# Kernel tuning notes

Hardware: AMD Instinct MI355X
Metric: run time of the kernel (lower is better)

Reference implementation:

```python
import jax, jax.numpy as jnp
import numpy as np

D_MODEL = 512
N_HEADS = 8
D_FF = 2048
E_LAYERS = 2
ENC_IN = 7
MARK_IN = 4
SEQ_LEN = 1536
PRED_LEN = 512
DEC_LEN = 768
BATCH = 8
BUCKET_SIZE = 4
N_HASHES = 4
L_TOTAL = SEQ_LEN + PRED_LEN  # 2048, multiple of 2*bucket_size
DH = D_MODEL // N_HEADS
N_BUCKETS = L_TOTAL // BUCKET_SIZE  # 512
SELF_ATTN_VALUE = -5e4  # reformer_pytorch TOKEN_SELF_ATTN_VALUE


def layernorm(x, g, b, eps=1e-5):
    mu = x.mean(-1, keepdims=True)
    var = ((x - mu) ** 2).mean(-1, keepdims=True)
    return (x - mu) * jax.lax.rsqrt(var + eps) * g + b


def lsh_attention(qk, v, rotations):
    # qk, v: [BH, L, dh]; rotations: [dh, n_hashes, n_buckets//2]
    BH, L, dh = qk.shape
    # --- hashing: argmax over [rotated, -rotated] ---
    rotated = jnp.einsum('bld,dhr->bhlr', qk, rotations)
    rotated = jnp.concatenate([rotated, -rotated], axis=-1)          # [BH,nh,L,nb]
    buckets = jnp.argmax(rotated, axis=-1).astype(jnp.int32)         # [BH,nh,L]
    offsets = (jnp.arange(N_HASHES, dtype=jnp.int32) * N_BUCKETS)[None, :, None]
    buckets = (buckets + offsets).reshape(BH, N_HASHES * L)
    # --- sort by (bucket, time) ---
    ticker = jnp.arange(N_HASHES * L, dtype=jnp.int32)
    buckets_and_t = buckets * L + (ticker % L)
    sticker = jnp.argsort(buckets_and_t, axis=-1).astype(jnp.int32)  # stable
    undo_sort = jnp.argsort(sticker, axis=-1)
    st = sticker % L                                                 # original positions
    sqk = jnp.take_along_axis(qk, st[..., None], axis=1)
    sv = jnp.take_along_axis(v, st[..., None], axis=1)
    # --- chunk: n_chunks = n_hashes * n_buckets, bucket_size per chunk ---
    n_chunks = N_HASHES * N_BUCKETS
    bq_t = st.reshape(BH, n_chunks, BUCKET_SIZE)
    bqk = sqk.reshape(BH, n_chunks, BUCKET_SIZE, dh)
    bv = sv.reshape(BH, n_chunks, BUCKET_SIZE, dh)
    bq = bqk
    bk = bqk / jnp.maximum(jnp.linalg.norm(bqk, axis=-1, keepdims=True), 1e-12)
    look = lambda x: jnp.concatenate([x, jnp.roll(x, 1, axis=1)], axis=2)  # look one chunk back
    bk, bve, bkv_t = look(bk), look(bv), look(bq_t)
    dots = jnp.einsum('bcie,bcje->bcij', bq, bk) * (dh ** -0.5)
    self_mask = bq_t[:, :, :, None] == bkv_t[:, :, None, :]
    dots = jnp.where(self_mask, SELF_ATTN_VALUE, dots)
    lse = jax.nn.logsumexp(dots, axis=-1, keepdims=True)
    probs = jnp.exp(dots - lse)
    bo = jnp.einsum('bcij,bcje->bcie', probs, bve)
    # --- unsort and combine hash rounds via logit weighting ---
    so = bo.reshape(BH, N_HASHES * L, dh)
    slog = lse.reshape(BH, N_HASHES * L)
    o = jnp.take_along_axis(so, undo_sort[..., None], axis=1)
    logits = jnp.take_along_axis(slog, undo_sort, axis=1)
    o = o.reshape(BH, N_HASHES, L, dh)
    logits = logits.reshape(BH, N_HASHES, L, 1)
    w = jax.nn.softmax(logits, axis=1)
    return (o * w).sum(axis=1)  # [BH, L, dh]


def split_heads(x, B, L):
    return x.reshape(B, L, N_HEADS, DH).transpose(0, 2, 1, 3).reshape(B * N_HEADS, L, DH)


def _forward(x_enc, x_mark_enc, x_dec, x_mark_dec, token_w, temp_w, qk_w, v_w, out_w, out_b,
             ln1_g, ln1_b, ff1_w, ff1_b, ff2_w, ff2_b, ln2_g, ln2_b, norm_g, norm_b,
             proj_w, proj_b, rotations):
    x = jnp.concatenate([x_enc, x_dec[:, -PRED_LEN:, :]], axis=1)        # [B,L,enc_in]
    xm = jnp.concatenate([x_mark_enc, x_mark_dec[:, -PRED_LEN:, :]], axis=1)
    B, L, _ = x.shape
    # TokenEmbedding: Conv1d(enc_in, d_model, k=3, circular, no bias)
    xp = jnp.concatenate([x[:, -1:], x, x[:, :1]], axis=1)               # circular pad 1
    val = sum(jnp.einsum('blc,dc->bld', xp[:, k:k + L], token_w[:, :, k]) for k in range(3))
    # PositionalEmbedding (sinusoidal)
    pos = jnp.arange(L, dtype=jnp.float32)[:, None]
    div = jnp.exp(jnp.arange(0, D_MODEL, 2, dtype=jnp.float32) * (-np.log(10000.0) / D_MODEL))
    pe = jnp.zeros((L, D_MODEL), jnp.float32)
    pe = pe.at[:, 0::2].set(jnp.sin(pos * div)).at[:, 1::2].set(jnp.cos(pos * div))
    # TimeFeatureEmbedding: Linear(4, d_model, no bias)
    h = val + xm @ temp_w.T + pe[None]
    for l in range(E_LAYERS):
        qk = split_heads(h @ qk_w[l].T, B, L)
        v = split_heads(h @ v_w[l].T, B, L)
        attn = lsh_attention(qk, v, rotations[l])
        attn = attn.reshape(B, N_HEADS, L, DH).transpose(0, 2, 1, 3).reshape(B, L, D_MODEL)
        attn = attn @ out_w[l].T + out_b[l]
        h = h + attn
        y = h = layernorm(h, ln1_g[l], ln1_b[l])
        y = jax.nn.gelu(y @ ff1_w[l].T + ff1_b[l], approximate=False)
        y = y @ ff2_w[l].T + ff2_b[l]
        h = layernorm(h + y, ln2_g[l], ln2_b[l])
    h = layernorm(h, norm_g, norm_b)
    dec_out = h @ proj_w.T + proj_b                                      # [B, L, 1]
    return dec_out[:, -PRED_LEN:][..., None]                             # [B, pred_len, 1, 1]


def setup_inputs() -> dict:
    key = jax.random.key(0)
    ks = iter(jax.random.split(key, 32))
    rn = lambda shape, s=0.02: jax.random.normal(next(ks), shape, jnp.float32) * s
    inp = {
        'x_enc': jax.random.normal(next(ks), (BATCH, SEQ_LEN, ENC_IN), jnp.float32),
        'x_mark_enc': jax.random.normal(next(ks), (BATCH, SEQ_LEN, MARK_IN), jnp.float32),
        'x_dec': jax.random.normal(next(ks), (BATCH, DEC_LEN, ENC_IN), jnp.float32),
        'x_mark_dec': jax.random.normal(next(ks), (BATCH, DEC_LEN, MARK_IN), jnp.float32),
        'token_w': rn((D_MODEL, ENC_IN, 3), 0.1),
        'temp_w': rn((D_MODEL, MARK_IN), 0.1),
        'qk_w': rn((E_LAYERS, D_MODEL, D_MODEL)),
        'v_w': rn((E_LAYERS, D_MODEL, D_MODEL)),
        'out_w': rn((E_LAYERS, D_MODEL, D_MODEL)),
        'out_b': jnp.zeros((E_LAYERS, D_MODEL), jnp.float32),
        'ln1_g': jnp.ones((E_LAYERS, D_MODEL), jnp.float32),
        'ln1_b': jnp.zeros((E_LAYERS, D_MODEL), jnp.float32),
        'ff1_w': rn((E_LAYERS, D_FF, D_MODEL)),
        'ff1_b': jnp.zeros((E_LAYERS, D_FF), jnp.float32),
        'ff2_w': rn((E_LAYERS, D_MODEL, D_FF)),
        'ff2_b': jnp.zeros((E_LAYERS, D_MODEL), jnp.float32),
        'ln2_g': jnp.ones((E_LAYERS, D_MODEL), jnp.float32),
        'ln2_b': jnp.zeros((E_LAYERS, D_MODEL), jnp.float32),
        'norm_g': jnp.ones((D_MODEL,), jnp.float32),
        'norm_b': jnp.zeros((D_MODEL,), jnp.float32),
        'proj_w': rn((1, D_MODEL)),
        'proj_b': jnp.zeros((1,), jnp.float32),
        'rotations': jax.random.normal(next(ks), (E_LAYERS, DH, N_HASHES, N_BUCKETS // 2), jnp.float32),
    }
    return inp


def reference(x_enc, x_mark_enc, x_dec, x_mark_dec, token_w, temp_w, qk_w, v_w, out_w, out_b,
              ln1_g, ln1_b, ff1_w, ff1_b, ff2_w, ff2_b, ln2_g, ln2_b, norm_g, norm_b,
              proj_w, proj_b, rotations):
    return _forward(x_enc, x_mark_enc, x_dec, x_mark_dec, token_w, temp_w, qk_w, v_w, out_w, out_b,
                    ln1_g, ln1_b, ff1_w, ff1_b, ff2_w, ff2_b, ln2_g, ln2_b, norm_g, norm_b,
                    proj_w, proj_b, rotations)
```

## Files before the change

kernel.cpp:

```cpp
#include <hip/hip_runtime.h>
#include <math.h>

#define BATCH 8
#define LTOT 2048
#define DM 512
#define NHEADS 8
#define DH 64
#define NBH 64
#define NHASH 4
#define SEQ 1536
#define DECL 768
#define DFF 2048
#define NCH 2048

typedef unsigned short u16;
typedef unsigned int u32;
typedef unsigned long long u64;
typedef __attribute__((ext_vector_type(8))) short short8;
typedef __attribute__((ext_vector_type(4))) float floatx4;

static __device__ __forceinline__ double gelu_d(double x) {
    return 0.5 * x * (1.0 + erf(x * 0.70710678118654752440));
}

static __device__ __forceinline__ u16 f2bf(float x) {
    u32 u = __float_as_uint(x);
    return (u16)((u + 0x7fffu + ((u >> 16) & 1u)) >> 16);
}
static __device__ __forceinline__ float bf2f(u16 h) {
    return __uint_as_float(((u32)h) << 16);
}
static __device__ __forceinline__ void split3(float x, u16& h, u16& m, u16& l) {
    h = f2bf(x);
    float r1 = x - bf2f(h);
    m = f2bf(r1);
    l = f2bf(r1 - bf2f(m));
}
static __device__ __forceinline__ u32 ordf(float x) {
    u32 b = __float_as_uint(x);
    return (b & 0x80000000u) ? ~b : (b | 0x80000000u);
}
static __device__ __forceinline__ u32 pack_hi16(u32 a, u32 b) {
    return __builtin_amdgcn_perm(b, a, 0x07060302u);
}
static __device__ __forceinline__ void tsplit3_pack(
    float x0, float x1, u32& ph, u32& pm, u32& pl)
{
    u32 b0 = __float_as_uint(x0), b1 = __float_as_uint(x1);
    ph = pack_hi16(b0, b1);
    float r0 = x0 - __uint_as_float(b0 & 0xFFFF0000u);
    float r1 = x1 - __uint_as_float(b1 & 0xFFFF0000u);
    u32 c0 = __float_as_uint(r0), c1 = __float_as_uint(r1);
    pm = pack_hi16(c0, c1);
    float s0 = r0 - __uint_as_float(c0 & 0xFFFF0000u);
    float s1 = r1 - __uint_as_float(c1 & 0xFFFF0000u);
    pl = pack_hi16(__float_as_uint(s0), __float_as_uint(s1));
}
static __device__ __forceinline__ void tsplit2_pack(
    float x0, float x1, u32& ph, u32& pm)
{
    u32 b0 = __float_as_uint(x0), b1 = __float_as_uint(x1);
    ph = pack_hi16(b0, b1);
    float r0 = x0 - __uint_as_float(b0 & 0xFFFF0000u);
    float r1 = x1 - __uint_as_float(b1 & 0xFFFF0000u);
    pm = pack_hi16(__float_as_uint(r0), __float_as_uint(r1));
}

__global__ __launch_bounds__(512) void build_h_kernel(
    const float* __restrict__ x_enc, const float* __restrict__ x_mark_enc,
    const float* __restrict__ x_dec, const float* __restrict__ x_mark_dec,
    const float* __restrict__ token_w, const float* __restrict__ temp_w,
    float* __restrict__ H)
{
    int bl = blockIdx.x;
    int b = bl >> 11, l = bl & 2047;
    __shared__ float xr[3][7];
    __shared__ float xmr[4];
    int tid = threadIdx.x;
    if (tid < 21) {
        int k = tid / 7, c = tid % 7;
        int t = (l + k - 1 + LTOT) & 2047;
        float v;
        if (t < SEQ) v = x_enc[(b * SEQ + t) * 7 + c];
        else         v = x_dec[(b * DECL + (t - 1280)) * 7 + c];
        xr[k][c] = v;
    } else if (tid < 25) {
        int m = tid - 21;
        float v;
        if (l < SEQ) v = x_mark_enc[(b * SEQ + l) * 4 + m];
        else         v = x_mark_dec[(b * DECL + (l - 1280)) * 4 + m];
        xmr[m] = v;
    }
    __syncthreads();
    int d = tid;
    double val = 0.0;
    #pragma unroll
    for (int k = 0; k < 3; ++k)
        #pragma unroll
        for (int c = 0; c < 7; ++c)
            val += (double)xr[k][c] * (double)token_w[(d * 7 + c) * 3 + k];
    double tmp = 0.0;
    #pragma unroll
    for (int m = 0; m < 4; ++m) tmp += (double)xmr[m] * (double)temp_w[d * 4 + m];
    const float cf = (float)(-9.210340371976184 / 512.0);
    float ef  = (float)(2 * (d >> 1)) * cf;
    float dvf = (float)exp((double)ef);
    float angf = (float)l * dvf;
    double pe = (d & 1) ? cos((double)angf) : sin((double)angf);
    H[((size_t)b * LTOT + l) * DM + d] = (float)(val + tmp + pe);
}

__global__ __launch_bounds__(256) void wsplit_kernel(
    const float* __restrict__ qkw, const float* __restrict__ vw,
    const float* __restrict__ ow, const float* __restrict__ f1w,
    const float* __restrict__ f2w,
    u16* __restrict__ Ph, u16* __restrict__ Pm, u16* __restrict__ Pl)
{
    size_t i = ((size_t)blockIdx.x * 256 + threadIdx.x) * 4;
    const float* src; size_t off, base; int kshift;
    if (i < 262144)       { src = qkw; off = i;           base = 0;       kshift = 9; }
    else if (i < 524288)  { src = vw;  off = i - 262144;  base = 262144;  kshift = 9; }
    else if (i < 786432)  { src = ow;  off = i - 524288;  base = 524288;  kshift = 9; }
    else if (i < 1835008) { src = f1w; off = i - 786432;  base = 786432;  kshift = 9; }
    else                  { src = f2w; off = i - 1835008; base = 1835008; kshift = 11; }
    int K = 1 << kshift;
    int n  = (int)(off >> kshift);
    int kg = (int)(off & (size_t)(K - 1));
    int nt = n >> 7, r = n & 127, kt = kg >> 5, kk = kg & 31;
    size_t o = base + ((((size_t)nt * (K >> 5) + kt) << 12) | ((size_t)r << 5) | kk);
    float4 x = *(const float4*)(src + off);
    u32 h01, m01, l01, h23, m23, l23;
    tsplit3_pack(x.x, x.y, h01, m01, l01);
    tsplit3_pack(x.z, x.w, h23, m23, l23);
    *(uint2*)(Ph + o) = make_uint2(h01, h23);
    *(uint2*)(Pm + o) = make_uint2(m01, m23);
    *(uint2*)(Pl + o) = make_uint2(l01, l23);
}

template<int NSPLIT>
__global__ __launch_bounds__(256) void gemm_mfma(
    const float* __restrict__ A,
    const u16* __restrict__ WTh, const u16* __restrict__ WTm,
    const u16* __restrict__ WTl,
    const float* __restrict__ bias, const float* __restrict__ res,
    float* __restrict__ C, int M, int N, int K, int act)
{
    __shared__ u16 Ah[128][32], Am[128][32], Al[128][32];
    __shared__ u16 Wh[128][32], Wm[128][32], Wl[128][32];
    const int tid = threadIdx.x;
    const int n0 = blockIdx.x * 128, m0 = blockIdx.y * 128;
    const int row = tid >> 1;
    const int koff = (tid & 1) * 16;
    const float* Ag = A + (size_t)(m0 + row) * K + koff;

    const int wv = tid >> 6, lane = tid & 63;
    const int m0w = (wv >> 1) * 64, n0w = (wv & 1) * 64;
    const int fr = lane & 15, quad = lane >> 4;
    u16* WhF = &Wh[0][0]; u16* WmF = &Wm[0][0]; u16* WlF = &Wl[0][0];

    floatx4 acc[4][4];
    #pragma unroll
    for (int i = 0; i < 4; ++i)
        #pragma unroll
        for (int j = 0; j < 4; ++j) acc[i][j] = (floatx4)0.0f;

    for (int kt = 0; kt < K; kt += 32) {
        const size_t tb = ((size_t)blockIdx.x * (K >> 5) + (kt >> 5)) * 4096;
        uint4 wh0 = *(const uint4*)(WTh + tb + tid * 8);
        uint4 wh1 = *(const uint4*)(WTh + tb + 2048 + tid * 8);
        uint4 wm0 = *(const uint4*)(WTm + tb + tid * 8);
        uint4 wm1 = *(const uint4*)(WTm + tb + 2048 + tid * 8);
        uint4 wl0, wl1;
        if (NSPLIT == 3) {
            wl0 = *(const uint4*)(WTl + tb + tid * 8);
            wl1 = *(const uint4*)(WTl + tb + 2048 + tid * 8);
        }
        u32 pah[8], pam[8], pal[8];
        #pragma unroll
        for (int g = 0; g < 4; ++g) {
            float4 a4 = *(const float4*)(Ag + kt + g * 4);
            if (NSPLIT == 3) {
                tsplit3_pack(a4.x, a4.y, pah[g*2], pam[g*2], pal[g*2]);
                tsplit3_pack(a4.z, a4.w, pah[g*2+1], pam[g*2+1], pal[g*2+1]);
            } else {
                tsplit2_pack(a4.x, a4.y, pah[g*2], pam[g*2]);
                tsplit2_pack(a4.z, a4.w, pah[g*2+1], pam[g*2+1]);
            }
        }
        __syncthreads();
        ((uint4*)&Ah[row][koff])[0] = make_uint4(pah[0], pah[1], pah[2], pah[3]);
        ((uint4*)&Ah[row][koff])[1] = make_uint4(pah[4], pah[5], pah[6], pah[7]);
        ((uint4*)&Am[row][koff])[0] = make_uint4(pam[0], pam[1], pam[2], pam[3]);
        ((uint4*)&Am[row][koff])[1] = make_uint4(pam[4], pam[5], pam[6], pam[7]);
        *(uint4*)(WhF + tid * 8) = wh0;
        *(uint4*)(WhF + 2048 + tid * 8) = wh1;
        *(uint4*)(WmF + tid * 8) = wm0;
        *(uint4*)(WmF + 2048 + tid * 8) = wm1;
        if (NSPLIT == 3) {
            ((uint4*)&Al[row][koff])[0] = make_uint4(pal[0], pal[1], pal[2], pal[3]);
            ((uint4*)&Al[row][koff])[1] = make_uint4(pal[4], pal[5], pal[6], pal[7]);
            *(uint4*)(WlF + tid * 8) = wl0;
            *(uint4*)(WlF + 2048 + tid * 8) = wl1;
        }
        __syncthreads();
        short8 ah4[4], am4[4], al4[4];
        #pragma unroll
        for (int rt = 0; rt < 4; ++rt) {
            int r = m0w + rt * 16 + fr;
            ah4[rt] = *(const short8*)&Ah[r][quad * 8];
            am4[rt] = *(const short8*)&Am[r][quad * 8];
            if (NSPLIT == 3) al4[rt] = *(const short8*)&Al[r][quad * 8];
        }
        #pragma unroll
        for (int ct = 0; ct < 4; ++ct) {
            int nrw = n0w + ct * 16 + fr;
            short8 bh4 = *(const short8*)&Wh[nrw][quad * 8];
            short8 bm4 = *(const short8*)&Wm[nrw][quad * 8];
            short8 bl4;
            if (NSPLIT == 3) bl4 = *(const short8*)&Wl[nrw][quad * 8];
            #pragma unroll
            for (int rt = 0; rt < 4; ++rt) {
                floatx4 c = acc[rt][ct];
                c = __builtin_amdgcn_mfma_f32_16x16x32_bf16(ah4[rt], bh4, c, 0, 0, 0);
                c = __builtin_amdgcn_mfma_f32_16x16x32_bf16(ah4[rt], bm4, c, 0, 0, 0);
                c = __builtin_amdgcn_mfma_f32_16x16x32_bf16(am4[rt], bh4, c, 0, 0, 0);
                if (NSPLIT == 3) {
                    c = __builtin_amdgcn_mfma_f32_16x16x32_bf16(ah4[rt], bl4, c, 0, 0, 0);
                    c = __builtin_amdgcn_mfma_f32_16x16x32_bf16(am4[rt], bm4, c, 0, 0, 0);
                    c = __builtin_amdgcn_mfma_f32_16x16x32_bf16(al4[rt], bh4, c, 0, 0, 0);
                }
                acc[rt][ct] = c;
            }
        }
    }
    #pragma unroll
    for (int rt = 0; rt < 4; ++rt) {
        #pragma unroll
        for (int ct = 0; ct < 4; ++ct) {
            int n = n0 + n0w + ct * 16 + fr;
            #pragma unroll
            for (int reg = 0; reg < 4; ++reg) {
                int m = m0 + m0w + rt * 16 + quad * 4 + reg;
                double v = (double)acc[rt][ct][reg];
                if (bias) v += (double)bias[n];
                if (res)  v += (double)res[(size_t)m * N + n];
                if (act == 1) v = gelu_d(v);
                C[(size_t)m * N + n] = (float)v;
            }
        }
    }
}

__global__ __launch_bounds__(256) void rot_split_kernel(
    const float* __restrict__ rot, u16* __restrict__ RSh,
    u16* __restrict__ RSm, u16* __restrict__ RSl)
{
    int h = blockIdx.x;
    int r = threadIdx.x;
    #pragma unroll 4
    for (int d = 0; d < 64; ++d) {
        float v = rot[(d * 4 + h) * 256 + r];
        u16 hh, mm, ll;
        split3(v, hh, mm, ll);
        size_t o = ((size_t)h * 256 + r) * 64 + d;
        RSh[o] = hh; RSm[o] = mm; RSl[o] = ll;
    }
}

__global__ __launch_bounds__(256) void lsh_hash_mfma(
    const float* __restrict__ QK, const u16* __restrict__ RSh,
    const u16* __restrict__ RSm, const u16* __restrict__ RSl,
    int* __restrict__ BKT)
{
    __shared__ u16 Ah[128][72], Am[128][72], Al[128][72];
    __shared__ u64 best[128];
    int bid = blockIdx.x;
    int tt = bid & 15;
    int h  = (bid >> 4) & 3;
    int bh = bid >> 6;
    int tid = threadIdx.x;
    int b = bh >> 3, hd = bh & 7;
    const int t0 = tt * 128;

    if (tid < 128) best[tid] = 0ull;

    {
        int row = tid >> 1;
        int kbase = (tid & 1) * 32;
        const float* src = QK + ((size_t)(b * LTOT + t0 + row)) * DM + hd * DH + kbase;
        u32 ph[16], pm[16], pl[16];
        #pragma unroll
        for (int g = 0; g < 8; ++g) {
            float4 a4 = *(const float4*)(src + g * 4);
            u16 h0, m0_, l0, h1, m1_, l1;
            split3(a4.x, h0, m0_, l0); split3(a4.y, h1, m1_, l1);
            ph[g*2]   = (u32)h0 | ((u32)h1 << 16);
            pm[g*2]   = (u32)m0_ | ((u32)m1_ << 16);
            pl[g*2]   = (u32)l0 | ((u32)l1 << 16);
            split3(a4.z, h0, m0_, l0); split3(a4.w, h1, m1_, l1);
            ph[g*2+1] = (u32)h0 | ((u32)h1 << 16);
            pm[g*2+1] = (u32)m0_ | ((u32)m1_ << 16);
            pl[g*2+1] = (u32)l0 | ((u32)l1 << 16);
        }
        #pragma unroll
        for (int g = 0; g < 4; ++g) {
            ((uint4*)&Ah[row][kbase])[g] = make_uint4(ph[g*4], ph[g*4+1], ph[g*4+2], ph[g*4+3]);
            ((uint4*)&Am[row][kbase])[g] = make_uint4(pm[g*4], pm[g*4+1], pm[g*4+2], pm[g*4+3]);
            ((uint4*)&Al[row][kbase])[g] = make_uint4(pl[g*4], pl[g*4+1], pl[g*4+2], pl[g*4+3]);
        }
    }
    __syncthreads();

    const int wv = tid >> 6, lane = tid & 63;
    const int fr = lane & 15, quad = lane >> 4;
    const int nbase = wv * 64;

    floatx4 acc[8][4];
    #pragma unroll
    for (int i = 0; i < 8; ++i)
        #pragma unroll
        for (int j = 0; j < 4; ++j) acc[i][j] = (floatx4)0.0f;

    #pragma unroll
    for (int kt = 0; kt < 2; ++kt) {
        #pragma unroll
        for (int ct = 0; ct < 4; ++ct) {
            size_t bo = ((size_t)h * 256 + nbase + ct * 16 + fr) * 64 + kt * 32 + quad * 8;
            short8 bh4 = *(const short8*)(RSh + bo);
            short8 bm4 = *(const short8*)(RSm + bo);
            short8 bl4 = *(const short8*)(RSl + bo);
            #pragma unroll
            for (int rt = 0; rt < 8; ++rt) {
                const int ar = rt * 16 + fr, ak = kt * 32 + quad * 8;
                short8 ah4 = *(const short8*)&Ah[ar][ak];
                short8 am4 = *(const short8*)&Am[ar][ak];
                short8 al4 = *(const short8*)&Al[ar][ak];
                floatx4 c = acc[rt][ct];
                c = __builtin_amdgcn_mfma_f32_16x16x32_bf16(ah4, bh4, c, 0, 0, 0);
                c = __builtin_amdgcn_mfma_f32_16x16x32_bf16(ah4, bm4, c, 0, 0, 0);
                c = __builtin_amdgcn_mfma_f32_16x16x32_bf16(am4, bh4, c, 0, 0, 0);
                c = __builtin_amdgcn_mfma_f32_16x16x32_bf16(ah4, bl4, c, 0, 0, 0);
                c = __builtin_amdgcn_mfma_f32_16x16x32_bf16(am4, bm4, c, 0, 0, 0);
                c = __builtin_amdgcn_mfma_f32_16x16x32_bf16(al4, bh4, c, 0, 0, 0);
                acc[rt][ct] = c;
            }
        }
    }

    #pragma unroll
    for (int rt = 0; rt < 8; ++rt) {
        #pragma unroll
        for (int reg = 0; reg < 4; ++reg) {
            u64 key = 0ull;
            #pragma unroll
            for (int ct = 0; ct < 4; ++ct) {
                float v = acc[rt][ct][reg];
                u32 idxp = nbase + ct * 16 + fr;
                u32 idxn = idxp + 256;
                u64 kp = ((u64)ordf(v) << 32) | (u32)(0xFFFFFFFFu - idxp);
                u64 kn = ((u64)ordf(-v) << 32) | (u32)(0xFFFFFFFFu - idxn);
                if (kp > key) key = kp;
                if (kn > key) key = kn;
            }
            #pragma unroll
            for (int m = 1; m <= 8; m <<= 1) {
                u64 o = __shfl_xor((unsigned long long)key, m, 64);
                if (o > key) key = o;
            }
            if (fr == 0) {
                int tok = rt * 16 + quad * 4 + reg;
                atomicMax(&best[tok], key);
            }
        }
    }
    __syncthreads();
    if (tid < 128) {
        u32 idx = 0xFFFFFFFFu - (u32)best[tid];
        BKT[((size_t)bh * NHASH + h) * LTOT + t0 + tid] = (int)idx;
    }
}

__global__ __launch_bounds__(256) void lsh_sort_kernel(
    const int* __restrict__ BKT, int* __restrict__ STS)
{
    __shared__ unsigned short bkt[2048];
    __shared__ unsigned int hist2[16][512];
    __shared__ unsigned int bstart[512];
    int bid = blockIdx.x;
    int h = bid & 3, bh = bid >> 2;
    int tid = threadIdx.x;
    const int* src = BKT + ((size_t)bh * NHASH + h) * LTOT;
    for (int t = tid; t < 2048; t += 256) bkt[t] = (unsigned short)src[t];
    for (int i = tid; i < 16 * 512; i += 256) (&hist2[0][0])[i] = 0u;
    __syncthreads();
    for (int t = tid; t < 2048; t += 256)
        atomicAdd(&hist2[t >> 7][bkt[t]], 1u);
    __syncthreads();
    for (int bb = tid; bb < 512; bb += 256) {
        unsigned int run = 0;
        #pragma unroll
        for (int g = 0; g < 16; ++g) {
            unsigned int c = hist2[g][bb];
            hist2[g][bb] = run;
            run += c;
        }
        bstart[bb] = run;
    }
    __syncthreads();
    if (tid == 0) {
        unsigned int run = 0;
        for (int bb = 0; bb < 512; ++bb) {
            unsigned int c = bstart[bb];
            bstart[bb] = run;
            run += c;
        }
    }
    __syncthreads();
    int* dst = STS + (size_t)bh * (NHASH * LTOT) + h * LTOT;
    for (int t = tid; t < 2048; t += 256) {
        int bb = bkt[t];
        unsigned int rank = hist2[t >> 7][bb];
        int g0 = t & ~127;
        for (int u = g0; u < t; ++u) rank += (bkt[u] == (unsigned short)bb);
        dst[bstart[bb] + rank] = t;
    }
}

__global__ __launch_bounds__(256) void attn_lse_kernel(
    const float* __restrict__ QK, const int* __restrict__ STS,
    float* __restrict__ LSE, float* __restrict__ PRB)
{
    int wid = (blockIdx.x * 256 + threadIdx.x) >> 6;
    int lane = threadIdx.x & 63;
    int bh = wid >> 11;
    int c  = wid & 2047;
    int cp = (c + NCH - 1) & (NCH - 1);
    const int* sts = STS + (size_t)bh * 8192;
    int tok[8];
    #pragma unroll
    for (int j = 0; j < 4; ++j) tok[j] = sts[4 * c + j];
    #pragma unroll
    for (int j = 0; j < 4; ++j) tok[4 + j] = sts[4 * cp + j];
    int b = bh >> 3, hd = bh & 7;
    const float* base = QK + ((size_t)b * LTOT) * DM + hd * DH + lane;
    float kd[8];
    #pragma unroll
    for (int j = 0; j < 8; ++j) kd[j] = base[(size_t)tok[j] * DM];
    float rnrm[8];
    #pragma unroll
    for (int j = 0; j < 8; ++j) {
        float v = kd[j] * kd[j];
        #pragma unroll
        for (int m = 32; m; m >>= 1) v += __shfl_xor(v, m, 64);
        rnrm[j] = 0.125f / fmaxf(sqrtf(v), 1e-12f);
    }
    int hr = c >> 9;
    size_t cbase = ((size_t)bh * NCH + c) * 32;
    float pkeep = 0.f;
    #pragma unroll
    for (int i = 0; i < 4; ++i) {
        float dots[8];
        float myd = -5e4f;
        #pragma unroll
        for (int j = 0; j < 8; ++j) {
            float v = kd[i] * kd[j];
            #pragma unroll
            for (int m = 32; m; m >>= 1) v += __shfl_xor(v, m, 64);
            dots[j] = (tok[j] == tok[i]) ? -5e4f : v * rnrm[j];
            if ((lane & 7) == j) myd = dots[j];
        }
        float mx = dots[0];
        #pragma unroll
        for (int j = 1; j < 8; ++j) mx = fmaxf(mx, dots[j]);
        float s = 0.f;
        #pragma unroll
        for (int j = 0; j < 8; ++j) s += expf(dots[j] - mx);
        float pn = expf(myd - mx) / s;
        if ((lane >> 3) == i) pkeep = pn;
        if (lane == 0)
            LSE[((size_t)bh * NHASH + hr) * LTOT + tok[i]] = mx + logf(s);
    }
    if (lane < 32) PRB[cbase + lane] = pkeep;
}

__global__ __launch_bounds__(256) void wsoft_kernel(
    const float* __restrict__ LSE, float* __restrict__ W4)
{
    int idx = blockIdx.x * 256 + threadIdx.x;
    int bh = idx >> 11, t = idx & 2047;
    float L[4];
    #pragma unroll
    for (int hh = 0; hh < 4; ++hh)
        L[hh] = LSE[((size_t)bh * NHASH + hh) * LTOT + t];
    float wm = fmaxf(fmaxf(L[0], L[1]), fmaxf(L[2], L[3]));
    float ws = 0.f;
    #pragma unroll
    for (int hh = 0; hh < 4; ++hh) ws += expf(L[hh] - wm);
    float inv = 1.f / ws;
    #pragma unroll
    for (int hh = 0; hh < 4; ++hh)
        W4[((size_t)bh * NHASH + hh) * LTOT + t] = expf(L[hh] - wm) * inv;
}

__global__ __launch_bounds__(256) void attn_out_kernel(
    const float* __restrict__ V, const int* __restrict__ STS,
    const float* __restrict__ PRB, const float* __restrict__ W4,
    float* __restrict__ C)
{
    int wid = (blockIdx.x * 256 + threadIdx.x) >> 6;
    int lane = threadIdx.x & 63;
    int bh = wid >> 11;
    int c  = wid & 2047;
    int cp = (c + NCH - 1) & (NCH - 1);
    const int* sts = STS + (size_t)bh * 8192;
    int tok[8];
    #pragma unroll
    for (int j = 0; j < 4; ++j) tok[j] = sts[4 * c + j];
    #pragma unroll
    for (int j = 0; j < 4; ++j) tok[4 + j] = sts[4 * cp + j];
    int b = bh >> 3, hd = bh & 7;
    const float* vbase = V + ((size_t)b * LTOT) * DM + hd * DH + lane;
    float vd[8];
    #pragma unroll
    for (int j = 0; j < 8; ++j) vd[j] = vbase[(size_t)tok[j] * DM];
    size_t cbase = ((size_t)bh * NCH + c) * 32;
    float pv = PRB[cbase + (lane & 31)];
    int hr = c >> 9;
    const float* w4b = W4 + ((size_t)bh * NHASH + hr) * LTOT;
    float* crow0 = C + ((size_t)b * LTOT) * DM + hd * DH + lane;
    #pragma unroll
    for (int i = 0; i < 4; ++i) {
        float w = w4b[tok[i]];
        float acc = 0.f;
        #pragma unroll
        for (int j = 0; j < 8; ++j)
            acc += __shfl(pv, i * 8 + j, 64) * vd[j];
        atomicAdd(crow0 + (size_t)tok[i] * DM, acc * w);
    }
}

__global__ __launch_bounds__(256) void ln_kernel(
    const float* __restrict__ X, float* __restrict__ Y,
    const float* __restrict__ g, const float* __restrict__ bta)
{
    int row = blockIdx.x;
    int tid = threadIdx.x;
    const float* x = X + (size_t)row * DM;
    double v0 = (double)x[tid], v1 = (double)x[tid + 256];
    double s = v0 + v1;
    double q = v0 * v0 + v1 * v1;
    #pragma unroll
    for (int off = 32; off; off >>= 1) {
        s += __shfl_down(s, off, 64);
        q += __shfl_down(q, off, 64);
    }
    __shared__ double ss[4], qq[4];
    int wid = tid >> 6, lane = tid & 63;
    if (lane == 0) { ss[wid] = s; qq[wid] = q; }
    __syncthreads();
    if (tid == 0) {
        double S = ss[0] + ss[1] + ss[2] + ss[3];
        double Q = qq[0] + qq[1] + qq[2] + qq[3];
        double mu = S * (1.0 / 512.0);
        double var = Q * (1.0 / 512.0) - mu * mu;
        ss[0] = mu;
        qq[0] = 1.0 / sqrt(var + 1e-5);
    }
    __syncthreads();
    double mu = ss[0], rs = qq[0];
    Y[(size_t)row * DM + tid] =
        (float)((v0 - mu) * rs * (double)g[tid] + (double)bta[tid]);
    Y[(size_t)row * DM + tid + 256] =
        (float)((v1 - mu) * rs * (double)g[tid + 256] + (double)bta[tid + 256]);
}

__global__ __launch_bounds__(64) void proj_kernel(
    const float* __restrict__ Hf, const float* __restrict__ pw,
    const float* __restrict__ pb, float* __restrict__ out)
{
    int idx = blockIdx.x;
    int b = idx >> 9, i = idx & 511;
    const float* row = Hf + ((size_t)(b * LTOT + SEQ + i)) * DM;
    int lane = threadIdx.x;
    double s = 0.0;
    #pragma unroll
    for (int k = 0; k < 8; ++k)
        s += (double)row[lane + 64 * k] * (double)pw[lane + 64 * k];
    #pragma unroll
    for (int off = 32; off; off >>= 1) s += __shfl_down(s, off, 64);
    if (lane == 0) out[idx] = (float)(s + (double)pb[0]);
}

extern "C" void kernel_launch(void* const* d_in, const int* in_sizes, int n_in,
                              void* d_out, int out_size, void* d_ws, size_t ws_size,
                              hipStream_t stream)
{
    const float* x_enc      = (const float*)d_in[0];
    const float* x_mark_enc = (const float*)d_in[1];
    const float* x_dec      = (const float*)d_in[2];
    const float* x_mark_dec = (const float*)d_in[3];
    const float* token_w    = (const float*)d_in[4];
    const float* temp_w     = (const float*)d_in[5];
    const float* qk_w       = (const float*)d_in[6];
    const float* v_w        = (const float*)d_in[7];
    const float* out_w      = (const float*)d_in[8];
    const float* out_b      = (const float*)d_in[9];
    const float* ln1_g      = (const float*)d_in[10];
    const float* ln1_b      = (const float*)d_in[11];
    const float* ff1_w      = (const float*)d_in[12];
    const float* ff1_b      = (const float*)d_in[13];
    const float* ff2_w      = (const float*)d_in[14];
    const float* ff2_b      = (const float*)d_in[15];
    const float* ln2_g      = (const float*)d_in[16];
    const float* ln2_b      = (const float*)d_in[17];
    const float* norm_g     = (const float*)d_in[18];
    const float* norm_b     = (const float*)d_in[19];
    const float* proj_w     = (const float*)d_in[20];
    const float* proj_b     = (const float*)d_in[21];
    const float* rotations  = (const float*)d_in[22];

    float* ws = (float*)d_ws;
    const size_t S = (size_t)BATCH * LTOT * DM;
    float* Hb  = ws;
    float* QKb = ws + S;
    float* Vb  = ws + 2 * S;
    float* Cb  = ws + 3 * S;
    float* Yb  = QKb;
    int*   BKTb = (int*)(ws + 4 * S);
    float* LSEb = ws + 4 * S + 524288;
    int*   STSb = (int*)(ws + 4 * S + 2 * 524288);
    u16*   RShb = (u16*)(ws + 4 * S + 3 * 524288);
    u16*   RSmb = RShb + 4 * 256 * 64;
    u16*   RSlb = RSmb + 4 * 256 * 64;
    const size_t WTOT = 2883584;
    u16*   WPh = (u16*)(ws + 4 * S + 3 * 524288 + 98304);
    u16*   WPm = WPh + WTOT;
    u16*   WPl = WPm + WTOT;
    float* PRBb = ws + 4 * S + 3 * 524288 + 98304 + (3 * WTOT) / 2;
    float* W4b  = PRBb + (size_t)NBH * NCH * 32;
    const size_t WO_QK = 0, WO_V = 262144, WO_O = 524288,
                 WO_F1 = 786432, WO_F2 = 1835008;

    build_h_kernel<<<BATCH * LTOT, 512, 0, stream>>>(
        x_enc, x_mark_enc, x_dec, x_mark_dec, token_w, temp_w, Hb);

    const int M = BATCH * LTOT;
    const int ATT_BLOCKS = NBH * NCH / 4;
    for (int l = 0; l < 2; ++l) {
        const float* qkw = qk_w + (size_t)l * DM * DM;
        const float* vw  = v_w  + (size_t)l * DM * DM;
        const float* ow  = out_w + (size_t)l * DM * DM;
        const float* ob  = out_b + (size_t)l * DM;
        const float* l1g = ln1_g + (size_t)l * DM;
        const float* l1b = ln1_b + (size_t)l * DM;
        const float* f1w = ff1_w + (size_t)l * DFF * DM;
        const float* f1b = ff1_b + (size_t)l * DFF;
        const float* f2w = ff2_w + (size_t)l * DM * DFF;
        const float* f2b = ff2_b + (size_t)l * DM;
        const float* l2g = ln2_g + (size_t)l * DM;
        const float* l2b = ln2_b + (size_t)l * DM;
        const float* rot = rotations + (size_t)l * DH * NHASH * 256;

        wsplit_kernel<<<2816, 256, 0, stream>>>(qkw, vw, ow, f1w, f2w, WPh, WPm, WPl);

        dim3 gQ(DM / 128, M / 128);
        gemm_mfma<3><<<gQ, 256, 0, stream>>>(Hb, WPh + WO_QK, WPm + WO_QK, WPl + WO_QK,
                                             nullptr, nullptr, QKb, M, DM, DM, 0);
        if (l == 0)
            gemm_mfma<3><<<gQ, 256, 0, stream>>>(Hb, WPh + WO_V, WPm + WO_V, WPl + WO_V,
                                                 nullptr, nullptr, Vb, M, DM, DM, 0);
        else
            gemm_mfma<2><<<gQ, 256, 0, stream>>>(Hb, WPh + WO_V, WPm + WO_V, WPl + WO_V,
                                                 nullptr, nullptr, Vb, M, DM, DM, 0);

        rot_split_kernel<<<4, 256, 0, stream>>>(rot, RShb, RSmb, RSlb);
        lsh_hash_mfma<<<NBH * NHASH * 16, 256, 0, stream>>>(QKb, RShb, RSmb, RSlb, BKTb);
        lsh_sort_kernel<<<NBH * NHASH, 256, 0, stream>>>(BKTb, STSb);

        hipMemsetAsync(Cb, 0, S * sizeof(float), stream);
        attn_lse_kernel<<<ATT_BLOCKS, 256, 0, stream>>>(QKb, STSb, LSEb, PRBb);
        wsoft_kernel<<<512, 256, 0, stream>>>(LSEb, W4b);
        attn_out_kernel<<<ATT_BLOCKS, 256, 0, stream>>>(Vb, STSb, PRBb, W4b, Cb);

        if (l == 0)
            gemm_mfma<3><<<gQ, 256, 0, stream>>>(Cb, WPh + WO_O, WPm + WO_O, WPl + WO_O,
                                                 ob, Hb, Hb, M, DM, DM, 0);
        else
            gemm_mfma<2><<<gQ, 256, 0, stream>>>(Cb, WPh + WO_O, WPm + WO_O, WPl + WO_O,
                                                 ob, Hb, Hb, M, DM, DM, 0);
        ln_kernel<<<M, 256, 0, stream>>>(Hb, Hb, l1g, l1b);

        for (int hb2 = 0; hb2 < 2; ++hb2) {
            float* hpart = Hb + (size_t)hb2 * 8192 * DM;
            dim3 gF1(DFF / 128, 8192 / 128);
            dim3 gF2(DM / 128, 8192 / 128);
            if (l == 0) {
                gemm_mfma<3><<<gF1, 256, 0, stream>>>(hpart, WPh + WO_F1, WPm + WO_F1, WPl + WO_F1,
                                                      f1b, nullptr, Yb, 8192, DFF, DM, 1);
                gemm_mfma<3><<<gF2, 256, 0, stream>>>(Yb, WPh + WO_F2, WPm + WO_F2, WPl + WO_F2,
                                                      f2b, hpart, hpart, 8192, DM, DFF, 0);
            } else {
                gemm_mfma<2><<<gF1, 256, 0, stream>>>(hpart, WPh + WO_F1, WPm + WO_F1, WPl + WO_F1,
                                                      f1b, nullptr, Yb, 8192, DFF, DM, 1);
                gemm_mfma<2><<<gF2, 256, 0, stream>>>(Yb, WPh + WO_F2, WPm + WO_F2, WPl + WO_F2,
                                                      f2b, hpart, hpart, 8192, DM, DFF, 0);
            }
        }
        ln_kernel<<<M, 256, 0, stream>>>(Hb, Hb, l2g, l2b);
    }

    ln_kernel<<<M, 256, 0, stream>>>(Hb, Cb, norm_g, norm_b);
    proj_kernel<<<4096, 64, 0, stream>>>(Cb, proj_w, proj_b, (float*)d_out);
}
```

Baseline: 3.335 ms.

## Split LSH hash accumulators into halves and precompute key norms

The hash kernel now processes its 128 rows in two halves of 64, which halves the accumulator register footprint. It also shrinks the LDS row padding and replaces the separate positive and negative argmax keys with a single key built from the magnitude and sign. Per-token key norms are computed once in a new kernel and read by the attention kernel, instead of being recomputed with shuffle reductions for all 8 keys in every chunk. The cost is one extra launch plus a small extra buffer read, and ties where the value is exactly zero may resolve differently.

```diff
diff --git a/kernel.cpp b/kernel.cpp
--- a/kernel.cpp
+++ b/kernel.cpp
@@ -272,7 +272,7 @@
     const u16* __restrict__ RSm, const u16* __restrict__ RSl,
     int* __restrict__ BKT)
 {
-    __shared__ u16 Ah[128][72], Am[128][72], Al[128][72];
+    __shared__ u16 Ah[128][68], Am[128][68], Al[128][68];
     __shared__ u64 best[128];
     int bid = blockIdx.x;
     int tt = bid & 15;
@@ -315,61 +315,63 @@
     const int fr = lane & 15, quad = lane >> 4;
     const int nbase = wv * 64;
 
-    floatx4 acc[8][4];
-    #pragma unroll
-    for (int i = 0; i < 8; ++i)
-        #pragma unroll
-        for (int j = 0; j < 4; ++j) acc[i][j] = (floatx4)0.0f;
-
-    #pragma unroll
-    for (int kt = 0; kt < 2; ++kt) {
-        #pragma unroll
-        for (int ct = 0; ct < 4; ++ct) {
-            size_t bo = ((size_t)h * 256 + nbase + ct * 16 + fr) * 64 + kt * 32 + quad * 8;
-            short8 bh4 = *(const short8*)(RSh + bo);
-            short8 bm4 = *(const short8*)(RSm + bo);
-            short8 bl4 = *(const short8*)(RSl + bo);
+    #pragma unroll
+    for (int half = 0; half < 2; ++half) {
+        floatx4 acc[4][4];
+        #pragma unroll
+        for (int i = 0; i < 4; ++i)
             #pragma unroll
-            for (int rt = 0; rt < 8; ++rt) {
-                const int ar = rt * 16 + fr, ak = kt * 32 + quad * 8;
-                short8 ah4 = *(const short8*)&Ah[ar][ak];
-                short8 am4 = *(const short8*)&Am[ar][ak];
-                short8 al4 = *(const short8*)&Al[ar][ak];
-                floatx4 c = acc[rt][ct];
-                c = __builtin_amdgcn_mfma_f32_16x16x32_bf16(ah4, bh4, c, 0, 0, 0);
-                c = __builtin_amdgcn_mfma_f32_16x16x32_bf16(ah4, bm4, c, 0, 0, 0);
-                c = __builtin_amdgcn_mfma_f32_16x16x32_bf16(am4, bh4, c, 0, 0, 0);
-                c = __builtin_amdgcn_mfma_f32_16x16x32_bf16(ah4, bl4, c, 0, 0, 0);
-                c = __builtin_amdgcn_mfma_f32_16x16x32_bf16(am4, bm4, c, 0, 0, 0);
-                c = __builtin_amdgcn_mfma_f32_16x16x32_bf16(al4, bh4, c, 0, 0, 0);
-                acc[rt][ct] = c;
-            }
-        }
-    }
-
-    #pragma unroll
-    for (int rt = 0; rt < 8; ++rt) {
-        #pragma unroll
-        for (int reg = 0; reg < 4; ++reg) {
-            u64 key = 0ull;
+            for (int j = 0; j < 4; ++j) acc[i][j] = (floatx4)0.0f;
+
+        #pragma unroll
+        for (int kt = 0; kt < 2; ++kt) {
             #pragma unroll
             for (int ct = 0; ct < 4; ++ct) {
-                float v = acc[rt][ct][reg];
-                u32 idxp = nbase + ct * 16 + fr;
-                u32 idxn = idxp + 256;
-                u64 kp = ((u64)ordf(v) << 32) | (u32)(0xFFFFFFFFu - idxp);
-                u64 kn = ((u64)ordf(-v) << 32) | (u32)(0xFFFFFFFFu - idxn);
-                if (kp > key) key = kp;
-                if (kn > key) key = kn;
+                size_t bo = ((size_t)h * 256 + nbase + ct * 16 + fr) * 64 + kt * 32 + quad * 8;
+                short8 bh4 = *(const short8*)(RSh + bo);
+                short8 bm4 = *(const short8*)(RSm + bo);
+                short8 bl4 = *(const short8*)(RSl + bo);
+                #pragma unroll
+                for (int rt = 0; rt < 4; ++rt) {
+                    const int ar = (half * 4 + rt) * 16 + fr, ak = kt * 32 + quad * 8;
+                    short8 ah4 = *(const short8*)&Ah[ar][ak];
+                    short8 am4 = *(const short8*)&Am[ar][ak];
+                    short8 al4 = *(const short8*)&Al[ar][ak];
+                    floatx4 c = acc[rt][ct];
+                    c = __builtin_amdgcn_mfma_f32_16x16x32_bf16(ah4, bh4, c, 0, 0, 0);
+                    c = __builtin_amdgcn_mfma_f32_16x16x32_bf16(ah4, bm4, c, 0, 0, 0);
+                    c = __builtin_amdgcn_mfma_f32_16x16x32_bf16(am4, bh4, c, 0, 0, 0);
+                    c = __builtin_amdgcn_mfma_f32_16x16x32_bf16(ah4, bl4, c, 0, 0, 0);
+                    c = __builtin_amdgcn_mfma_f32_16x16x32_bf16(am4, bm4, c, 0, 0, 0);
+                    c = __builtin_amdgcn_mfma_f32_16x16x32_bf16(al4, bh4, c, 0, 0, 0);
+                    acc[rt][ct] = c;
+                }
             }
+        }
+
+        #pragma unroll
+        for (int rt = 0; rt < 4; ++rt) {
             #pragma unroll
-            for (int m = 1; m <= 8; m <<= 1) {
-                u64 o = __shfl_xor((unsigned long long)key, m, 64);
-                if (o > key) key = o;
-            }
-            if (fr == 0) {
-                int tok = rt * 16 + quad * 4 + reg;
-                atomicMax(&best[tok], key);
+            for (int reg = 0; reg < 4; ++reg) {
+                u64 key = 0ull;
+                #pragma unroll
+                for (int ct = 0; ct < 4; ++ct) {
+                    float v = acc[rt][ct][reg];
+                    float mag = fabsf(v);
+                    u32 idx = nbase + ct * 16 + fr + ((v >= 0.f) ? 0u : 256u);
+                    u64 k = ((u64)(__float_as_uint(mag) | 0x80000000u) << 32)
+                            | (u32)(0xFFFFFFFFu - idx);
+                    if (k > key) key = k;
+                }
+                #pragma unroll
+                for (int m = 1; m <= 8; m <<= 1) {
+                    u64 o = __shfl_xor((unsigned long long)key, m, 64);
+                    if (o > key) key = o;
+                }
+                if (fr == 0) {
+                    int tok = (half * 4 + rt) * 16 + quad * 4 + reg;
+                    atomicMax(&best[tok], key);
+                }
             }
         }
     }
@@ -426,8 +428,24 @@
     }
 }
 
+__global__ __launch_bounds__(256) void knorm_kernel(
+    const float* __restrict__ QK, float* __restrict__ RN)
+{
+    int wid = (blockIdx.x * 256 + threadIdx.x) >> 6;
+    int lane = threadIdx.x & 63;
+    int bh = wid >> 11, t = wid & 2047;
+    int b = bh >> 3, hd = bh & 7;
+    float kv = QK[((size_t)(b * LTOT + t)) * DM + hd * DH + lane];
+    float v = kv * kv;
+    #pragma unroll
+    for (int m = 32; m; m >>= 1) v += __shfl_xor(v, m, 64);
+    if (lane == 0)
+        RN[(size_t)bh * LTOT + t] = 0.125f / fmaxf(sqrtf(v), 1e-12f);
+}
+
 __global__ __launch_bounds__(256) void attn_lse_kernel(
     const float* __restrict__ QK, const int* __restrict__ STS,
+    const float* __restrict__ RN,
     float* __restrict__ LSE, float* __restrict__ PRB)
 {
     int wid = (blockIdx.x * 256 + threadIdx.x) >> 6;
@@ -446,14 +464,10 @@
     float kd[8];
     #pragma unroll
     for (int j = 0; j < 8; ++j) kd[j] = base[(size_t)tok[j] * DM];
+    const float* rnb = RN + (size_t)bh * LTOT;
     float rnrm[8];
     #pragma unroll
-    for (int j = 0; j < 8; ++j) {
-        float v = kd[j] * kd[j];
-        #pragma unroll
-        for (int m = 32; m; m >>= 1) v += __shfl_xor(v, m, 64);
-        rnrm[j] = 0.125f / fmaxf(sqrtf(v), 1e-12f);
-    }
+    for (int j = 0; j < 8; ++j) rnrm[j] = rnb[tok[j]];
     int hr = c >> 9;
     size_t cbase = ((size_t)bh * NCH + c) * 32;
     float pkeep = 0.f;
@@ -638,6 +652,7 @@
     u16*   WPl = WPm + WTOT;
     float* PRBb = ws + 4 * S + 3 * 524288 + 98304 + (3 * WTOT) / 2;
     float* W4b  = PRBb + (size_t)NBH * NCH * 32;
+    float* RNb  = W4b + (size_t)NBH * NHASH * LTOT;
     const size_t WO_QK = 0, WO_V = 262144, WO_O = 524288,
                  WO_F1 = 786432, WO_F2 = 1835008;
 
@@ -676,9 +691,10 @@
         rot_split_kernel<<<4, 256, 0, stream>>>(rot, RShb, RSmb, RSlb);
         lsh_hash_mfma<<<NBH * NHASH * 16, 256, 0, stream>>>(QKb, RShb, RSmb, RSlb, BKTb);
         lsh_sort_kernel<<<NBH * NHASH, 256, 0, stream>>>(BKTb, STSb);
+        knorm_kernel<<<32768, 256, 0, stream>>>(QKb, RNb);
 
         hipMemsetAsync(Cb, 0, S * sizeof(float), stream);
-        attn_lse_kernel<<<ATT_BLOCKS, 256, 0, stream>>>(QKb, STSb, LSEb, PRBb);
+        attn_lse_kernel<<<ATT_BLOCKS, 256, 0, stream>>>(QKb, STSb, RNb, LSEb, PRBb);
         wsoft_kernel<<<512, 256, 0, stream>>>(LSEb, W4b);
         attn_out_kernel<<<ATT_BLOCKS, 256, 0, stream>>>(Vb, STSb, PRBb, W4b, Cb);
 
```

After: 2.740 ms. -17.9%, faster.
